# Kernel tuning notes

Hardware: AMD Instinct MI355X
Metric: run time of the kernel (lower is better)

Reference implementation:

```python
import jax, jax.numpy as jnp
import numpy as np

N_TOKENS = 16384
MODEL_DIM = 2048
NUM_EXPERTS = 16
TOP_K = 2
CAPACITY_FACTOR = 1.0
NUM_SPLIT = 2  # os.environ 'num_split' default in source


def setup_inputs() -> dict:
    key = jax.random.key(0)
    kx, kw = jax.random.split(key)
    x = jax.random.normal(kx, (N_TOKENS, MODEL_DIM), dtype=jnp.float32)
    # kaiming_normal_ on Linear weight: std = sqrt(2 / fan_in)
    wg = jax.random.normal(kw, (NUM_EXPERTS, MODEL_DIM), dtype=jnp.float32) * np.float32(np.sqrt(2.0 / MODEL_DIM))
    return {"x": x, "wg": wg}


def _loss_compute(logits):
    gates = jax.nn.softmax(logits, axis=1)              # [N, E]
    num_experts = logits.shape[1]
    indices1_s = jnp.argmax(gates, axis=1)              # [N]
    mask1 = jax.nn.one_hot(indices1_s, num_experts, dtype=gates.dtype)
    me = jnp.mean(gates, axis=0)
    ce = jnp.mean(mask1, axis=0)
    l_aux = jnp.sum(me * ce) * num_experts
    return l_aux, indices1_s, gates


def _dispatch_fix_capacity(gates, k, capacity_factor, num_split):
    # gates is detached in the original (torch .detach())
    gates = jax.lax.stop_gradient(gates)
    n, e = gates.shape
    capacity = int(k * n // e * capacity_factor) // num_split * num_split
    values, topk_idx = jax.lax.top_k(gates, k)          # [N, k]
    weights = values
    flat_experts = topk_idx.reshape(-1)                 # [N*k]
    order = jnp.argsort(flat_experts)                   # stable sort by expert id
    experts_sorted = flat_experts[order]
    token_ids = jnp.repeat(jnp.arange(n, dtype=jnp.int32), k)[order]
    # position of each routed token within its expert's run
    counts = jax.ops.segment_sum(jnp.ones_like(flat_experts, dtype=jnp.int32), flat_experts, num_segments=e)
    starts = jnp.cumsum(counts) - counts                # exclusive prefix sum
    pos = jnp.arange(n * k, dtype=jnp.int32) - starts[experts_sorted]
    # fixed-capacity index table, -1 = empty slot; overflow tokens dropped
    ind = jnp.full((e, capacity), -1, dtype=jnp.int32)
    ind = ind.at[experts_sorted, pos].set(token_ids, mode="drop")  # pos>=capacity dropped
    indices = ind.reshape(-1)                           # [E*capacity], expert-major
    mask = indices >= 0
    expert_ids = jnp.repeat(jnp.arange(e, dtype=gates.dtype), capacity)
    return weights, indices, expert_ids, mask


def reference(x, wg):
    logits = jnp.einsum("nd,ed->ne", x, wg)             # Linear, no bias
    l_aux, _indices1, gates = _loss_compute(logits)
    weights, indices, expert_ids, mask = _dispatch_fix_capacity(
        gates, TOP_K, CAPACITY_FACTOR, NUM_SPLIT)
    return l_aux, weights, indices, expert_ids
```

## Files before the change

kernel.cpp:

```cpp
#include <hip/hip_runtime.h>
#include <hip/hip_bf16.h>
#include <stdint.h>

#define N_TOKENS    16384
#define MODEL_DIM   2048
#define NUM_EXPERTS 16
#define CAPACITY    2048
#define NBLK        256
#define GBLK        512
#define W_OFF       1
#define IDX_OFF     (1 + 2 * N_TOKENS)
#define EID_OFF     (IDX_OFF + NUM_EXPERTS * CAPACITY)

#define SCR_BYTE  (4 * EID_OFF)
#define SC_E01    0
#define SC_CNT    16384
#define SC_START  24576
#define SC_CE2    32768

__global__ __launch_bounds__(512) void k_logits(
    const float* __restrict__ x, const float* __restrict__ wg,
    float* __restrict__ out, float* __restrict__ me, uint8_t* __restrict__ scr)
{
  __shared__ float part[8][32][17];
  const int tid = threadIdx.x;
  const int b = blockIdx.x;
  const int l = tid & 63;
  const int kr = tid >> 6;
  const int kb = kr * 256 + l * 4;

  float4 w[16];
#pragma unroll
  for (int e = 0; e < NUM_EXPERTS; ++e)
    w[e] = *reinterpret_cast<const float4*>(wg + e * MODEL_DIM + kb);

  const float* xp = x + (size_t)(b * 32) * MODEL_DIM + kb;
  float4 xva = *reinterpret_cast<const float4*>(xp);

  for (int t = 0; t < 32; ++t) {
    float4 xvb;
    if (t < 31)
      xvb = *reinterpret_cast<const float4*>(xp + (size_t)(t + 1) * MODEL_DIM);

    float cur[16];
#pragma unroll
    for (int e = 0; e < NUM_EXPERTS; ++e)
      cur[e] = xva.x * w[e].x + xva.y * w[e].y + xva.z * w[e].z + xva.w * w[e].w;

#pragma unroll
    for (int s = 0; s < 4; ++s) {
      const int d = 1 << s;
      const bool hi = (l >> s) & 1;
#pragma unroll
      for (int r = 0; r < (16 >> (s + 1)); ++r) {
        float keep  = hi ? cur[2 * r + 1] : cur[2 * r];
        float other = hi ? cur[2 * r]     : cur[2 * r + 1];
        cur[r] = keep + __shfl_xor(other, d, 64);
      }
    }
    float v = cur[0];
    v += __shfl_xor(v, 16, 64);
    v += __shfl_xor(v, 32, 64);
    if (l < NUM_EXPERTS) part[kr][t][l] = v;
    xva = xvb;
  }
  __syncthreads();

  if (tid < 32) {
    const int tg = b * 32 + tid;
    float logit[NUM_EXPERTS];
#pragma unroll
    for (int e = 0; e < NUM_EXPERTS; ++e) {
      float s = part[0][tid][e];
#pragma unroll
      for (int k2 = 1; k2 < 8; ++k2) s += part[k2][tid][e];
      logit[e] = s;
    }

    float m = logit[0];
#pragma unroll
    for (int e = 1; e < NUM_EXPERTS; e++) m = fmaxf(m, logit[e]);
    float gg[NUM_EXPERTS]; float z = 0.f;
#pragma unroll
    for (int e = 0; e < NUM_EXPERTS; e++) { gg[e] = expf(logit[e] - m); z += gg[e]; }
    float inv = 1.f / z;
#pragma unroll
    for (int e = 0; e < NUM_EXPERTS; e++) gg[e] *= inv;

    float v1 = gg[0], v2 = -1.f; int e1 = 0, e2 = 0;
#pragma unroll
    for (int e = 1; e < NUM_EXPERTS; e++) {
      if (gg[e] > v1) { v2 = v1; e2 = e1; v1 = gg[e]; e1 = e; }
      else if (gg[e] > v2) { v2 = gg[e]; e2 = e; }
    }
    out[W_OFF + 2 * tg]     = v1;
    out[W_OFF + 2 * tg + 1] = v2;
    scr[SC_E01 + tg] = (uint8_t)(e1 | (e2 << 4));

#pragma unroll
    for (int e = 0; e < NUM_EXPERTS; e++) {
      gg[e] += __shfl_xor(gg[e], 1, 64);
      gg[e] += __shfl_xor(gg[e], 2, 64);
      gg[e] += __shfl_xor(gg[e], 4, 64);
      gg[e] += __shfl_xor(gg[e], 8, 64);
      gg[e] += __shfl_xor(gg[e], 16, 64);
    }
    if (tid == 0) {
#pragma unroll
      for (int e = 0; e < NUM_EXPERTS; e++) me[b * NUM_EXPERTS + e] = gg[e];
    }
  }
}

__global__ __launch_bounds__(64) void k_route(
    const uint8_t* __restrict__ scr_ro, uint8_t* __restrict__ scr) {
  const int c = blockIdx.x;
  const int lane = threadIdx.x;
  const int v = scr_ro[SC_E01 + c * 64 + lane];
  const int e1 = v & 15, e2 = v >> 4;
  int mycount = 0, myce = 0;
  for (int e = 0; e < NUM_EXPERTS; e++) {
    unsigned long long m1 = __ballot(e1 == e);
    unsigned long long m2 = __ballot(e2 == e);
    if (lane == e) { mycount = __popcll(m1 | m2); myce = __popcll(m1); }
  }
  if (lane < NUM_EXPERTS) {
    reinterpret_cast<uint16_t*>(scr + SC_CNT)[lane * NBLK + c] = (uint16_t)mycount;
    reinterpret_cast<uint16_t*>(scr + SC_CE2)[lane * NBLK + c] = (uint16_t)myce;
  }
}

__global__ __launch_bounds__(256) void k_finish(
    uint8_t* __restrict__ scr, const float* __restrict__ me,
    float* __restrict__ out) {
  const uint16_t* counts = reinterpret_cast<const uint16_t*>(scr + SC_CNT);
  uint16_t* starts = reinterpret_cast<uint16_t*>(scr + SC_START);
  __shared__ int gs[NUM_EXPERTS][16];
  __shared__ int gstart[NUM_EXPERTS][17];
  __shared__ float sme[NUM_EXPERTS][17];
  __shared__ int sce[NUM_EXPERTS][17];
  const int tid = threadIdx.x;
  const int e = tid >> 4, grp = tid & 15;
  int s = 0;
  for (int c = grp * 16; c < grp * 16 + 16; c++) s += counts[e * NBLK + c];
  gs[e][grp] = s;
  {
    const uint16_t* ce2 = reinterpret_cast<const uint16_t*>(scr + SC_CE2);
    float ms = 0.f;
    for (int k = grp; k < GBLK; k += 16) ms += me[k * NUM_EXPERTS + e];
    int cs = 0;
    for (int k = grp; k < NBLK; k += 16) cs += ce2[e * NBLK + k];
    sme[e][grp] = ms; sce[e][grp] = cs;
  }
  __syncthreads();
  if (tid < NUM_EXPERTS) {
    int run = 0;
    for (int g2 = 0; g2 < 16; g2++) { gstart[tid][g2] = run; run += gs[tid][g2]; }
  }
  __syncthreads();
  int run = gstart[e][grp];
  for (int c = grp * 16; c < grp * 16 + 16; c++) {
    starts[e * NBLK + c] = (uint16_t)run;
    run += counts[e * NBLK + c];
  }
  if (tid < NUM_EXPERTS) {
    float ssum = 0.f; int ce = 0;
    for (int g2 = 0; g2 < 16; g2++) { ssum += sme[tid][g2]; ce += sce[tid][g2]; }
    float prod = (ssum * (1.0f / N_TOKENS)) * ((float)ce * (1.0f / N_TOKENS));
    prod += __shfl_xor(prod, 1, 64);
    prod += __shfl_xor(prod, 2, 64);
    prod += __shfl_xor(prod, 4, 64);
    prod += __shfl_xor(prod, 8, 64);
    if (tid == 0) out[0] = prod * (float)NUM_EXPERTS;
  }
}

__global__ __launch_bounds__(64) void k_scatter(
    const uint8_t* __restrict__ scr, float* __restrict__ out) {
  const uint16_t* starts = reinterpret_cast<const uint16_t*>(scr + SC_START);
  const int c = blockIdx.x;
  const int lane = threadIdx.x;
  const int t = c * 64 + lane;
  const int v = scr[SC_E01 + t];
  const int e1 = v & 15, e2 = v >> 4;
  const unsigned long long below = (1ull << lane) - 1ull;
  int p1 = CAPACITY, p2 = CAPACITY;
  for (int e = 0; e < NUM_EXPERTS; e++) {
    unsigned long long m = __ballot(e1 == e) | __ballot(e2 == e);
    int r = __popcll(m & below);
    int sbase = (int)starts[e * NBLK + c];
    if (e1 == e) p1 = sbase + r;
    if (e2 == e) p2 = sbase + r;
  }
  float tf = (float)t;
  if ((unsigned)p1 < (unsigned)CAPACITY) out[IDX_OFF + e1 * CAPACITY + p1] = tf;
  if ((unsigned)p2 < (unsigned)CAPACITY) out[IDX_OFF + e2 * CAPACITY + p2] = tf;
}

__global__ __launch_bounds__(256) void k_fill_idx(
    const uint8_t* __restrict__ scr, float* __restrict__ out) {
  const uint16_t* counts = reinterpret_cast<const uint16_t*>(scr + SC_CNT);
  const uint16_t* starts = reinterpret_cast<const uint16_t*>(scr + SC_START);
  const int i = blockIdx.x * 256 + threadIdx.x;
  const int e = i >> 11;
  const int p = i & (CAPACITY - 1);
  const int tot = (int)starts[e * NBLK + NBLK - 1] + (int)counts[e * NBLK + NBLK - 1];
  if (p >= tot) out[IDX_OFF + i] = -1.0f;
}

__global__ __launch_bounds__(256) void k_eid(float* __restrict__ out) {
  const int i = blockIdx.x * 256 + threadIdx.x;
  out[EID_OFF + i] = (float)(i >> 11);
}

extern "C" void kernel_launch(void* const* d_in, const int* in_sizes, int n_in,
                              void* d_out, int out_size, void* d_ws, size_t ws_size,
                              hipStream_t stream) {
  const float* x  = (const float*)d_in[0];
  const float* wg = (const float*)d_in[1];
  float* out = (float*)d_out;
  uint8_t* scr = (uint8_t*)d_out + SCR_BYTE;
  float* me = out + IDX_OFF;
  (void)d_ws; (void)ws_size;

  k_logits<<<GBLK, 512, 0, stream>>>(x, wg, out, me, scr);
  k_route<<<NBLK, 64, 0, stream>>>(scr, scr);
  k_finish<<<1, 256, 0, stream>>>(scr, me, out);
  k_scatter<<<NBLK, 64, 0, stream>>>(scr, out);
  k_fill_idx<<<128, 256, 0, stream>>>(scr, out);
  k_eid<<<128, 256, 0, stream>>>(out);
}
```

Baseline: 58.04 us.

## Fuse routing kernels into logits and merge scatter/fill/eid; use DPP reductions

Folds the per-block expert counting into the logits kernel (per 32-token half-block), merges scatter, -1 fill and expert-id writes into one kernel, and moves scratch from the output buffer into the workspace. The cross-lane reduction in the logits dot product switches from generic shuffles to DPP and ds_swizzle intrinsics. This cuts kernel launches from six to three and lowers reduction latency. The cost is more work in the single-block finish kernel and a tighter coupling of the count layout between kernels.

```diff
diff --git a/kernel.cpp b/kernel.cpp
--- a/kernel.cpp
+++ b/kernel.cpp
@@ -6,21 +6,28 @@
 #define MODEL_DIM   2048
 #define NUM_EXPERTS 16
 #define CAPACITY    2048
+#define NBLK2       512
 #define NBLK        256
 #define GBLK        512
 #define W_OFF       1
 #define IDX_OFF     (1 + 2 * N_TOKENS)
 #define EID_OFF     (IDX_OFF + NUM_EXPERTS * CAPACITY)
 
-#define SCR_BYTE  (4 * EID_OFF)
 #define SC_E01    0
-#define SC_CNT    16384
-#define SC_START  24576
-#define SC_CE2    32768
+#define SC_CNTH   16384
+#define SC_CEH    32768
+#define SC_START  49152
+#define SC_TOT    57344
+#define SC_ME     57408
+
+#define DPPX(v, ctrl) __int_as_float(__builtin_amdgcn_update_dpp(             \
+    0, __float_as_int(v), (ctrl), 0xF, 0xF, true))
+#define SWZ(v, off) __int_as_float(__builtin_amdgcn_ds_swizzle(               \
+    __float_as_int(v), (off)))
 
 __global__ __launch_bounds__(512) void k_logits(
     const float* __restrict__ x, const float* __restrict__ wg,
-    float* __restrict__ out, float* __restrict__ me, uint8_t* __restrict__ scr)
+    float* __restrict__ out, uint8_t* __restrict__ ws)
 {
   __shared__ float part[8][32][17];
   const int tid = threadIdx.x;
@@ -37,6 +44,8 @@
   const float* xp = x + (size_t)(b * 32) * MODEL_DIM + kb;
   float4 xva = *reinterpret_cast<const float4*>(xp);
 
+  const bool h0 = l & 1, h1 = l & 2, h2 = l & 4, h3 = l & 8;
+
   for (int t = 0; t < 32; ++t) {
     float4 xvb;
     if (t < 31)
@@ -48,18 +57,30 @@
       cur[e] = xva.x * w[e].x + xva.y * w[e].y + xva.z * w[e].z + xva.w * w[e].w;
 
 #pragma unroll
-    for (int s = 0; s < 4; ++s) {
-      const int d = 1 << s;
-      const bool hi = (l >> s) & 1;
-#pragma unroll
-      for (int r = 0; r < (16 >> (s + 1)); ++r) {
-        float keep  = hi ? cur[2 * r + 1] : cur[2 * r];
-        float other = hi ? cur[2 * r]     : cur[2 * r + 1];
-        cur[r] = keep + __shfl_xor(other, d, 64);
-      }
-    }
-    float v = cur[0];
-    v += __shfl_xor(v, 16, 64);
+    for (int r = 0; r < 8; ++r) {
+      float k = h0 ? cur[2 * r + 1] : cur[2 * r];
+      float o = h0 ? cur[2 * r]     : cur[2 * r + 1];
+      cur[r] = k + DPPX(o, 0xB1);
+    }
+#pragma unroll
+    for (int r = 0; r < 4; ++r) {
+      float k = h1 ? cur[2 * r + 1] : cur[2 * r];
+      float o = h1 ? cur[2 * r]     : cur[2 * r + 1];
+      cur[r] = k + DPPX(o, 0x4E);
+    }
+#pragma unroll
+    for (int r = 0; r < 2; ++r) {
+      float k = h2 ? cur[2 * r + 1] : cur[2 * r];
+      float o = h2 ? cur[2 * r]     : cur[2 * r + 1];
+      cur[r] = k + SWZ(o, 0x101F);
+    }
+    float v;
+    {
+      float k = h3 ? cur[1] : cur[0];
+      float o = h3 ? cur[0] : cur[1];
+      v = k + SWZ(o, 0x201F);
+    }
+    v += SWZ(v, 0x401F);
     v += __shfl_xor(v, 32, 64);
     if (l < NUM_EXPERTS) part[kr][t][l] = v;
     xva = xvb;
@@ -95,7 +116,18 @@
     }
     out[W_OFF + 2 * tg]     = v1;
     out[W_OFF + 2 * tg + 1] = v2;
-    scr[SC_E01 + tg] = (uint8_t)(e1 | (e2 << 4));
+    ws[SC_E01 + tg] = (uint8_t)(e1 | (e2 << 4));
+
+    int mycount = 0, myce = 0;
+    for (int e = 0; e < NUM_EXPERTS; e++) {
+      unsigned long long m1 = __ballot(e1 == e);
+      unsigned long long m2 = __ballot(e2 == e);
+      if (tid == e) { mycount = __popcll(m1 | m2); myce = __popcll(m1); }
+    }
+    if (tid < NUM_EXPERTS) {
+      reinterpret_cast<uint16_t*>(ws + SC_CNTH)[tid * NBLK2 + b] = (uint16_t)mycount;
+      reinterpret_cast<uint16_t*>(ws + SC_CEH)[tid * NBLK2 + b] = (uint16_t)myce;
+    }
 
 #pragma unroll
     for (int e = 0; e < NUM_EXPERTS; e++) {
@@ -106,35 +138,18 @@
       gg[e] += __shfl_xor(gg[e], 16, 64);
     }
     if (tid == 0) {
-#pragma unroll
-      for (int e = 0; e < NUM_EXPERTS; e++) me[b * NUM_EXPERTS + e] = gg[e];
-    }
-  }
-}
-
-__global__ __launch_bounds__(64) void k_route(
-    const uint8_t* __restrict__ scr_ro, uint8_t* __restrict__ scr) {
-  const int c = blockIdx.x;
-  const int lane = threadIdx.x;
-  const int v = scr_ro[SC_E01 + c * 64 + lane];
-  const int e1 = v & 15, e2 = v >> 4;
-  int mycount = 0, myce = 0;
-  for (int e = 0; e < NUM_EXPERTS; e++) {
-    unsigned long long m1 = __ballot(e1 == e);
-    unsigned long long m2 = __ballot(e2 == e);
-    if (lane == e) { mycount = __popcll(m1 | m2); myce = __popcll(m1); }
-  }
-  if (lane < NUM_EXPERTS) {
-    reinterpret_cast<uint16_t*>(scr + SC_CNT)[lane * NBLK + c] = (uint16_t)mycount;
-    reinterpret_cast<uint16_t*>(scr + SC_CE2)[lane * NBLK + c] = (uint16_t)myce;
+      float* mp = reinterpret_cast<float*>(ws + SC_ME);
+#pragma unroll
+      for (int e = 0; e < NUM_EXPERTS; e++) mp[b * NUM_EXPERTS + e] = gg[e];
+    }
   }
 }
 
 __global__ __launch_bounds__(256) void k_finish(
-    uint8_t* __restrict__ scr, const float* __restrict__ me,
-    float* __restrict__ out) {
-  const uint16_t* counts = reinterpret_cast<const uint16_t*>(scr + SC_CNT);
-  uint16_t* starts = reinterpret_cast<uint16_t*>(scr + SC_START);
+    uint8_t* __restrict__ ws, float* __restrict__ out) {
+  const uint16_t* cnth = reinterpret_cast<const uint16_t*>(ws + SC_CNTH);
+  uint16_t* starts = reinterpret_cast<uint16_t*>(ws + SC_START);
+  uint16_t* totw = reinterpret_cast<uint16_t*>(ws + SC_TOT);
   __shared__ int gs[NUM_EXPERTS][16];
   __shared__ int gstart[NUM_EXPERTS][17];
   __shared__ float sme[NUM_EXPERTS][17];
@@ -142,14 +157,16 @@
   const int tid = threadIdx.x;
   const int e = tid >> 4, grp = tid & 15;
   int s = 0;
-  for (int c = grp * 16; c < grp * 16 + 16; c++) s += counts[e * NBLK + c];
+  for (int hc = grp * 32; hc < grp * 32 + 32; hc++) s += cnth[e * NBLK2 + hc];
   gs[e][grp] = s;
   {
-    const uint16_t* ce2 = reinterpret_cast<const uint16_t*>(scr + SC_CE2);
-    float ms = 0.f;
-    for (int k = grp; k < GBLK; k += 16) ms += me[k * NUM_EXPERTS + e];
-    int cs = 0;
-    for (int k = grp; k < NBLK; k += 16) cs += ce2[e * NBLK + k];
+    const float* mepart = reinterpret_cast<const float*>(ws + SC_ME);
+    const uint16_t* ceh = reinterpret_cast<const uint16_t*>(ws + SC_CEH);
+    float ms = 0.f; int cs = 0;
+    for (int k = grp; k < NBLK2; k += 16) {
+      ms += mepart[k * NUM_EXPERTS + e];
+      cs += ceh[e * NBLK2 + k];
+    }
     sme[e][grp] = ms; sce[e][grp] = cs;
   }
   __syncthreads();
@@ -161,8 +178,9 @@
   int run = gstart[e][grp];
   for (int c = grp * 16; c < grp * 16 + 16; c++) {
     starts[e * NBLK + c] = (uint16_t)run;
-    run += counts[e * NBLK + c];
-  }
+    run += cnth[e * NBLK2 + 2 * c] + cnth[e * NBLK2 + 2 * c + 1];
+  }
+  if (grp == 15) totw[e] = (uint16_t)run;
   if (tid < NUM_EXPERTS) {
     float ssum = 0.f; int ce = 0;
     for (int g2 = 0; g2 < 16; g2++) { ssum += sme[tid][g2]; ce += sce[tid][g2]; }
@@ -175,42 +193,35 @@
   }
 }
 
-__global__ __launch_bounds__(64) void k_scatter(
-    const uint8_t* __restrict__ scr, float* __restrict__ out) {
-  const uint16_t* starts = reinterpret_cast<const uint16_t*>(scr + SC_START);
-  const int c = blockIdx.x;
-  const int lane = threadIdx.x;
-  const int t = c * 64 + lane;
-  const int v = scr[SC_E01 + t];
-  const int e1 = v & 15, e2 = v >> 4;
-  const unsigned long long below = (1ull << lane) - 1ull;
-  int p1 = CAPACITY, p2 = CAPACITY;
-  for (int e = 0; e < NUM_EXPERTS; e++) {
-    unsigned long long m = __ballot(e1 == e) | __ballot(e2 == e);
-    int r = __popcll(m & below);
-    int sbase = (int)starts[e * NBLK + c];
-    if (e1 == e) p1 = sbase + r;
-    if (e2 == e) p2 = sbase + r;
-  }
-  float tf = (float)t;
-  if ((unsigned)p1 < (unsigned)CAPACITY) out[IDX_OFF + e1 * CAPACITY + p1] = tf;
-  if ((unsigned)p2 < (unsigned)CAPACITY) out[IDX_OFF + e2 * CAPACITY + p2] = tf;
-}
-
-__global__ __launch_bounds__(256) void k_fill_idx(
-    const uint8_t* __restrict__ scr, float* __restrict__ out) {
-  const uint16_t* counts = reinterpret_cast<const uint16_t*>(scr + SC_CNT);
-  const uint16_t* starts = reinterpret_cast<const uint16_t*>(scr + SC_START);
-  const int i = blockIdx.x * 256 + threadIdx.x;
-  const int e = i >> 11;
-  const int p = i & (CAPACITY - 1);
-  const int tot = (int)starts[e * NBLK + NBLK - 1] + (int)counts[e * NBLK + NBLK - 1];
-  if (p >= tot) out[IDX_OFF + i] = -1.0f;
-}
-
-__global__ __launch_bounds__(256) void k_eid(float* __restrict__ out) {
-  const int i = blockIdx.x * 256 + threadIdx.x;
-  out[EID_OFF + i] = (float)(i >> 11);
+__global__ __launch_bounds__(192) void k_scatter_fill(
+    const uint8_t* __restrict__ ws, float* __restrict__ out) {
+  const uint16_t* starts = reinterpret_cast<const uint16_t*>(ws + SC_START);
+  const uint16_t* totw = reinterpret_cast<const uint16_t*>(ws + SC_TOT);
+  const int tid = threadIdx.x;
+  const int b = blockIdx.x;
+  if (tid < 64) {
+    const int t = b * 64 + tid;
+    const int v = ws[SC_E01 + t];
+    const int e1 = v & 15, e2 = v >> 4;
+    const unsigned long long below = (1ull << tid) - 1ull;
+    int p1 = CAPACITY, p2 = CAPACITY;
+    for (int e = 0; e < NUM_EXPERTS; e++) {
+      unsigned long long m = __ballot(e1 == e) | __ballot(e2 == e);
+      int r = __popcll(m & below);
+      int sbase = (int)starts[e * NBLK + b];
+      if (e1 == e) p1 = sbase + r;
+      if (e2 == e) p2 = sbase + r;
+    }
+    float tf = (float)t;
+    if ((unsigned)p1 < (unsigned)CAPACITY) out[IDX_OFF + e1 * CAPACITY + p1] = tf;
+    if ((unsigned)p2 < (unsigned)CAPACITY) out[IDX_OFF + e2 * CAPACITY + p2] = tf;
+  } else {
+    const int slot = b * 128 + (tid - 64);
+    const int e = slot >> 11;
+    const int p = slot & (CAPACITY - 1);
+    if (p >= (int)totw[e]) out[IDX_OFF + slot] = -1.0f;
+    out[EID_OFF + slot] = (float)e;
+  }
 }
 
 extern "C" void kernel_launch(void* const* d_in, const int* in_sizes, int n_in,
@@ -219,14 +230,9 @@
   const float* x  = (const float*)d_in[0];
   const float* wg = (const float*)d_in[1];
   float* out = (float*)d_out;
-  uint8_t* scr = (uint8_t*)d_out + SCR_BYTE;
-  float* me = out + IDX_OFF;
-  (void)d_ws; (void)ws_size;
-
-  k_logits<<<GBLK, 512, 0, stream>>>(x, wg, out, me, scr);
-  k_route<<<NBLK, 64, 0, stream>>>(scr, scr);
-  k_finish<<<1, 256, 0, stream>>>(scr, me, out);
-  k_scatter<<<NBLK, 64, 0, stream>>>(scr, out);
-  k_fill_idx<<<128, 256, 0, stream>>>(scr, out);
-  k_eid<<<128, 256, 0, stream>>>(out);
-}
+  uint8_t* ws = (uint8_t*)d_ws;
+
+  k_logits<<<GBLK, 512, 0, stream>>>(x, wg, out, ws);
+  k_finish<<<1, 256, 0, stream>>>(ws, out);
+  k_scatter_fill<<<NBLK, 192, 0, stream>>>(ws, out);
+}
```

Result: faster. 52.11 us (-10.2%).
